# Optimization experiments

Measured on AMD Instinct MI355X. Metric: run time of the kernel, lower is better.

## Reference

```python
import jax, jax.numpy as jnp
import jax.scipy.linalg
import numpy as np
import math

IMG = 512
PATCH = 14
NDIM = 2
HEAD_DIM = 128  # dim // heads = 4096 // 32
STEPS = math.ceil(IMG / PATCH)  # 37


def setup_inputs() -> dict:
    key = jax.random.key(0)
    k1, = jax.random.split(key, 1)
    gen = jax.random.uniform(k1, (NDIM, 1, HEAD_DIM, HEAD_DIM), dtype=jnp.float32) * (2.0 * math.pi)
    image_sizes = jnp.full((1, NDIM), IMG, dtype=jnp.int32)
    return {"image_sizes": image_sizes, "generator_raw_params": gen}


def _positions():
    # cartesian product of linspace(0,1,STEPS) along each axis -> [1, STEPS**NDIM, NDIM]
    axes = [jnp.linspace(0.0, 1.0, STEPS, dtype=jnp.float32) for _ in range(NDIM)]
    grid = jnp.stack(jnp.meshgrid(*axes, indexing="ij"), axis=-1).reshape(-1, NDIM)
    return grid[None]  # [1, N, NDIM]


def reference(image_sizes, generator_raw_params):
    positions = _positions()  # [1, N, NDIM]; image size is static (512) per jit requirements
    upper = jnp.triu(generator_raw_params, k=1) - 0.5  # [NDIM,1,D,D]
    skew = upper - jnp.swapaxes(upper, -1, -2)          # skew-symmetric bases
    # sum over input dims: generator per position, [1, N, 1, D, D]
    gen_pos = jnp.einsum("bnd,dhij->bnhij", positions, skew)
    cls = jnp.zeros_like(gen_pos[:, :1])                # CLS token generator (identity rotation)
    gen_pos = jnp.concatenate([cls, gen_pos], axis=1)   # [1, N+1, 1, D, D]
    b, n, h, d, _ = gen_pos.shape
    flat = gen_pos.astype(jnp.float32).reshape(b * n * h, d, d)
    rot = jax.vmap(jax.scipy.linalg.expm)(flat)
    return rot.reshape(b, n, h, d, d).astype(positions.dtype)
```

## Files before the change

kernel.cpp:

```cpp
#include <hip/hip_runtime.h>
#include <math.h>

#define STEPS 37
#define NMAT  (STEPS*STEPS + 1)
#define D     128
#define NT    512

typedef _Float16 half8 __attribute__((ext_vector_type(8)));
typedef __fp16   fp16x2 __attribute__((ext_vector_type(2)));
typedef float    f32x4 __attribute__((ext_vector_type(4)));

#define PH_OFF   0
#define PL_OFF   32768
#define QTH_OFF  65536
#define QTL_OFF  98304
#define RED_OFF  131072
#define LDS_BYTES (131072 + 640)

__constant__ float dC[8] = {
    1.0f, 1.0f, 5.0e-1f, 1.6666666666666666e-1f, 4.1666666666666664e-2f,
    8.3333333333333332e-3f, 1.3888888888888889e-3f, 1.9841269841269841e-4f };

template<bool WQT, bool WXR, bool WGL>
__device__ __forceinline__ void matmul_step(unsigned char* sm, float diagc,
                                            float* __restrict__ gout,
                                            int wr, int wc, int lr, int g)
{
    f32x4 acc1[4][2] = {};
    f32x4 acc2[4][2] = {};

    #pragma unroll
    for (int ks = 0; ks < 4; ++ks) {
        const int slot = 4*ks + g;
        half8 ah[4], al[4];
        #pragma unroll
        for (int bi = 0; bi < 4; ++bi) {
            const int r = wr*64 + bi*16 + lr;
            const int off = r*256 + ((slot ^ (r & 7)) << 4);
            ah[bi] = *(const half8*)(sm + PH_OFF + off);
            al[bi] = *(const half8*)(sm + PL_OFF + off);
        }
        #pragma unroll
        for (int bj = 0; bj < 2; ++bj) {
            const int c = wc*32 + bj*16 + lr;
            const int off = c*256 + ((slot ^ (c & 7)) << 4);
            const half8 qh = *(const half8*)(sm + QTH_OFF + off);
            const half8 ql = *(const half8*)(sm + QTL_OFF + off);
            #pragma unroll
            for (int bi = 0; bi < 4; ++bi) {
                acc1[bi][bj] = __builtin_amdgcn_mfma_f32_16x16x32_f16(ah[bi], qh, acc1[bi][bj], 0, 0, 0);
                acc2[bi][bj] = __builtin_amdgcn_mfma_f32_16x16x32_f16(ah[bi], ql, acc2[bi][bj], 0, 0, 0);
                acc2[bi][bj] = __builtin_amdgcn_mfma_f32_16x16x32_f16(al[bi], qh, acc2[bi][bj], 0, 0, 0);
            }
        }
    }

    if (WGL) {
        #pragma unroll
        for (int bi = 0; bi < 4; ++bi)
            #pragma unroll
            for (int bj = 0; bj < 2; ++bj) {
                const int col = wc*32 + bj*16 + lr;
                const int r0  = wr*64 + bi*16 + 4*g;
                #pragma unroll
                for (int q = 0; q < 4; ++q)
                    gout[(r0+q)*D + col] = acc1[bi][bj][q] + acc2[bi][bj][q] * (1.0f/2048.0f);
            }
        return;
    }

    uint2 uhv[4][2], ulv[4][2];
    #pragma unroll
    for (int bi = 0; bi < 4; ++bi) {
        #pragma unroll
        for (int bj = 0; bj < 2; ++bj) {
            const int col = wc*32 + bj*16 + lr;
            const int r0  = wr*64 + bi*16 + 4*g;
            float v[4];
            #pragma unroll
            for (int q = 0; q < 4; ++q)
                v[q] = acc1[bi][bj][q] + acc2[bi][bj][q] * (1.0f/2048.0f);
            if (wr*64 + bi*16 == wc*32 + bj*16) {
                #pragma unroll
                for (int q = 0; q < 4; ++q)
                    if (r0 + q == col) v[q] += diagc;
            }
            const fp16x2 h01 = __builtin_amdgcn_cvt_pkrtz(v[0], v[1]);
            const fp16x2 h23 = __builtin_amdgcn_cvt_pkrtz(v[2], v[3]);
            const fp16x2 l01 = __builtin_amdgcn_cvt_pkrtz((v[0]-(float)h01[0])*2048.f,
                                                          (v[1]-(float)h01[1])*2048.f);
            const fp16x2 l23 = __builtin_amdgcn_cvt_pkrtz((v[2]-(float)h23[0])*2048.f,
                                                          (v[3]-(float)h23[1])*2048.f);
            union { fp16x2 h2[2]; uint2 u; } cvh, cvl;
            cvh.h2[0] = h01; cvh.h2[1] = h23;
            cvl.h2[0] = l01; cvl.h2[1] = l23;
            uhv[bi][bj] = cvh.u; ulv[bi][bj] = cvl.u;
        }
    }
    __syncthreads();

    #pragma unroll
    for (int bi = 0; bi < 4; ++bi) {
        #pragma unroll
        for (int bj = 0; bj < 2; ++bj) {
            const int col = wc*32 + bj*16 + lr;
            const int r0  = wr*64 + bi*16 + 4*g;
            if (WQT) {
                const int off = col*256 + (((r0 >> 3) ^ (col & 7)) << 4) + ((g & 1) << 3);
                *(uint2*)(sm + QTH_OFF + off) = uhv[bi][bj];
                *(uint2*)(sm + QTL_OFF + off) = ulv[bi][bj];
            }
            if (WXR) {
                union { uint2 u; _Float16 h[4]; } th, tl;
                th.u = uhv[bi][bj]; tl.u = ulv[bi][bj];
                #pragma unroll
                for (int q = 0; q < 4; ++q) {
                    const int rr = r0 + q;
                    const int off = rr*256 + ((((col >> 3) ^ (rr & 7))) << 4) + ((col & 7) << 1);
                    *(_Float16*)(sm + PH_OFF + off) = th.h[q];
                    *(_Float16*)(sm + PL_OFF + off) = tl.h[q];
                }
            }
        }
    }
    __syncthreads();
}

__global__ __launch_bounds__(NT, 1)
void liere_expm_mfma(const float* __restrict__ gen, float* __restrict__ out)
{
    __shared__ __align__(16) unsigned char sm[LDS_BYTES];
    const int tid = threadIdx.x;
    const int wg  = blockIdx.x;

    float px = 0.f, py = 0.f;
    if (wg > 0) {
        const int idx = wg - 1;
        px = (float)(idx / STEPS) * (1.0f/(STEPS-1));
        py = (float)(idx % STEPS) * (1.0f/(STEPS-1));
    }

    float* Gp = (float*)sm;
    const float* g0 = gen;
    const float* g1 = gen + D*D;
    for (int it = 0; it < 32; ++it) {
        const int e = tid + (it << 9);
        const int i = e >> 7, j = e & 127;
        if (i < j) {
            const float v = px*g0[e] + py*g1[e];
            Gp[i*132 + j] =  v;
            Gp[j*132 + i] = -v;
        } else if (i == j) {
            Gp[i*132 + j] = 0.f;
        }
    }
    __syncthreads();

    float* red = (float*)(sm + RED_OFF);
    if (tid < D) {
        float s = 0.f;
        const f32x4* rowp = (const f32x4*)&Gp[tid*132];
        #pragma unroll 8
        for (int u = 0; u < 32; ++u) {
            const f32x4 v = rowp[u];
            s += fabsf(v.x) + fabsf(v.y) + fabsf(v.z) + fabsf(v.w);
        }
        red[tid] = s;
    }
    __syncthreads();
    #pragma unroll
    for (int off = 64; off >= 1; off >>= 1) {
        if (tid < off) red[tid] = fmaxf(red[tid], red[tid + off]);
        __syncthreads();
    }
    const float m = red[0];
    int nsq = 0;
    if (m > 0.5f) nsq = (int)ceilf(log2f(m * 2.0f));
    if (nsq < 0) nsq = 0;
    const float scale = exp2f(-(float)nsq);

    float vst[32];
    #pragma unroll
    for (int it = 0; it < 32; ++it) {
        const int e = tid + (it << 9);
        vst[it] = Gp[(e>>7)*132 + (e&127)];
    }
    __syncthreads();

    {
        const float c7 = dC[7], c6 = dC[6];
        #pragma unroll
        for (int it = 0; it < 32; ++it) {
            const int e = tid + (it << 9);
            const int i = e >> 7, j = e & 127;
            const float p = vst[it] * scale;
            const _Float16 ph = (_Float16)p;
            const _Float16 pl = (_Float16)((p - (float)ph) * 2048.f);
            const int offP = i*256 + (((j >> 3) ^ (i & 7)) << 4) + ((j & 7) << 1);
            *(_Float16*)(sm + PH_OFF + offP) = ph;
            *(_Float16*)(sm + PL_OFF + offP) = pl;
            const float x = c7*p + ((i == j) ? c6 : 0.f);
            const _Float16 xh = (_Float16)x;
            const _Float16 xl = (_Float16)((x - (float)xh) * 2048.f);
            const int offQ = j*256 + (((i >> 3) ^ (j & 7)) << 4) + ((i & 7) << 1);
            *(_Float16*)(sm + QTH_OFF + offQ) = xh;
            *(_Float16*)(sm + QTL_OFF + offQ) = xl;
        }
    }
    __syncthreads();

    const int lid = tid & 63;
    const int wid = tid >> 6;
    const int wr = wid >> 2, wc = wid & 3;
    const int lr = lid & 15, g = lid >> 4;
    float* gout = out + (size_t)wg * (D*D);

    for (int kk = 5; kk >= 1; --kk)
        matmul_step<true, false, false>(sm, dC[kk], gout, wr, wc, lr, g);
    matmul_step<true, true, false>(sm, dC[0], gout, wr, wc, lr, g);

    if (nsq == 0) {
        for (int it = 0; it < 32; ++it) {
            const int e = tid + (it << 9);
            const int i = e >> 7, j = e & 127;
            const int off = i*256 + (((j >> 3) ^ (i & 7)) << 4) + ((j & 7) << 1);
            gout[e] = (float)*(_Float16*)(sm + PH_OFF + off)
                    + (float)*(_Float16*)(sm + PL_OFF + off) * (1.0f/2048.0f);
        }
        return;
    }

    for (int t = 0; t < nsq - 1; ++t)
        matmul_step<true, true, false>(sm, 0.f, gout, wr, wc, lr, g);
    matmul_step<false, false, true>(sm, 0.f, gout, wr, wc, lr, g);
}

extern "C" void kernel_launch(void* const* d_in, const int* in_sizes, int n_in,
                              void* d_out, int out_size, void* d_ws, size_t ws_size,
                              hipStream_t stream) {
    (void)in_sizes; (void)n_in; (void)d_ws; (void)ws_size; (void)out_size;
    const float* gen = (const float*)d_in[1];
    float* out = (float*)d_out;
    liere_expm_mfma<<<NMAT, NT, 0, stream>>>(gen, out);
}
```

Before: 465.6 us.

## Use 1024-thread blocks, keep P in registers, and ping-pong Horner buffers

Doubles the block to 16 waves, so each wave computes a 32x32 output tile instead of 64x32. The scaled generator P is loaded once into registers and reused across all Horner steps, which removes the repeated LDS reads of the A operand. The Horner Q operand now alternates between two LDS buffers, which drops one barrier per step except the last. In exchange it raises thread count and register pressure per block, and each wave does less MFMA work per barrier.

```diff
diff --git a/kernel.cpp b/kernel.cpp
--- a/kernel.cpp
+++ b/kernel.cpp
@@ -4,129 +4,188 @@
 #define STEPS 37
 #define NMAT  (STEPS*STEPS + 1)
 #define D     128
-#define NT    512
+#define NT    1024
 
 typedef _Float16 half8 __attribute__((ext_vector_type(8)));
 typedef __fp16   fp16x2 __attribute__((ext_vector_type(2)));
 typedef float    f32x4 __attribute__((ext_vector_type(4)));
 
-#define PH_OFF   0
-#define PL_OFF   32768
-#define QTH_OFF  65536
-#define QTL_OFF  98304
-#define RED_OFF  131072
+#define R0H 0
+#define R0L 32768
+#define R1H 65536
+#define R1L 98304
+#define RED_OFF 131072
 #define LDS_BYTES (131072 + 640)
 
 __constant__ float dC[8] = {
     1.0f, 1.0f, 5.0e-1f, 1.6666666666666666e-1f, 4.1666666666666664e-2f,
     8.3333333333333332e-3f, 1.3888888888888889e-3f, 1.9841269841269841e-4f };
 
-template<bool WQT, bool WXR, bool WGL>
-__device__ __forceinline__ void matmul_step(unsigned char* sm, float diagc,
-                                            float* __restrict__ gout,
+__device__ __forceinline__ int swzA(int r, int slot) {
+    return r*256 + ((slot ^ (r & 7)) << 4);
+}
+__device__ __forceinline__ int swzE(int r, int c) {
+    return r*256 + (((c >> 3) ^ (r & 7)) << 4) + ((c & 7) << 1);
+}
+
+__device__ __forceinline__ void conv_tile(const f32x4 a1, const f32x4 a2,
+                                          float diagc, bool hasdiag,
+                                          int r0, int col, uint2& uh, uint2& ul)
+{
+    float v[4];
+    #pragma unroll
+    for (int q = 0; q < 4; ++q) v[q] = a1[q] + a2[q] * (1.0f/2048.0f);
+    if (hasdiag) {
+        #pragma unroll
+        for (int q = 0; q < 4; ++q) if (r0 + q == col) v[q] += diagc;
+    }
+    const fp16x2 h01 = __builtin_amdgcn_cvt_pkrtz(v[0], v[1]);
+    const fp16x2 h23 = __builtin_amdgcn_cvt_pkrtz(v[2], v[3]);
+    const fp16x2 l01 = __builtin_amdgcn_cvt_pkrtz((v[0]-(float)h01[0])*2048.f,
+                                                  (v[1]-(float)h01[1])*2048.f);
+    const fp16x2 l23 = __builtin_amdgcn_cvt_pkrtz((v[2]-(float)h23[0])*2048.f,
+                                                  (v[3]-(float)h23[1])*2048.f);
+    union { fp16x2 h2[2]; uint2 u; } ch, cl;
+    ch.h2[0] = h01; ch.h2[1] = h23;
+    cl.h2[0] = l01; cl.h2[1] = l23;
+    uh = ch.u; ul = cl.u;
+}
+
+template<bool LAST>
+__device__ __forceinline__ void horner_step(unsigned char* sm,
+                                            int srcH, int srcL, int dstH, int dstL,
+                                            const half8 (&pah)[2][4], const half8 (&pal)[2][4],
+                                            float diagc, int wr, int wc, int lr, int g)
+{
+    f32x4 acc1[2][2] = {};
+    f32x4 acc2[2][2] = {};
+    #pragma unroll
+    for (int ks = 0; ks < 4; ++ks) {
+        const int slot = 4*ks + g;
+        #pragma unroll
+        for (int bj = 0; bj < 2; ++bj) {
+            const int c = wc*32 + bj*16 + lr;
+            const int off = swzA(c, slot);
+            const half8 qh = *(const half8*)(sm + srcH + off);
+            const half8 ql = *(const half8*)(sm + srcL + off);
+            #pragma unroll
+            for (int bi = 0; bi < 2; ++bi) {
+                acc1[bi][bj] = __builtin_amdgcn_mfma_f32_16x16x32_f16(pah[bi][ks], qh, acc1[bi][bj], 0, 0, 0);
+                acc2[bi][bj] = __builtin_amdgcn_mfma_f32_16x16x32_f16(pah[bi][ks], ql, acc2[bi][bj], 0, 0, 0);
+                acc2[bi][bj] = __builtin_amdgcn_mfma_f32_16x16x32_f16(pal[bi][ks], qh, acc2[bi][bj], 0, 0, 0);
+            }
+        }
+    }
+    uint2 uh[2][2], ul[2][2];
+    #pragma unroll
+    for (int bi = 0; bi < 2; ++bi)
+        #pragma unroll
+        for (int bj = 0; bj < 2; ++bj) {
+            const int col = wc*32 + bj*16 + lr;
+            const int r0  = wr*32 + bi*16 + 4*g;
+            conv_tile(acc1[bi][bj], acc2[bi][bj], diagc,
+                      wr*32 + bi*16 == wc*32 + bj*16, r0, col, uh[bi][bj], ul[bi][bj]);
+        }
+    if (LAST) __syncthreads();
+    #pragma unroll
+    for (int bi = 0; bi < 2; ++bi)
+        #pragma unroll
+        for (int bj = 0; bj < 2; ++bj) {
+            const int col = wc*32 + bj*16 + lr;
+            const int r0  = wr*32 + bi*16 + 4*g;
+            const int offQ = col*256 + (((r0 >> 3) ^ (col & 7)) << 4) + ((g & 1) << 3);
+            *(uint2*)(sm + dstH + offQ) = uh[bi][bj];
+            *(uint2*)(sm + dstL + offQ) = ul[bi][bj];
+            if (LAST) {
+                union { uint2 u; _Float16 h[4]; } th, tl;
+                th.u = uh[bi][bj]; tl.u = ul[bi][bj];
+                #pragma unroll
+                for (int q = 0; q < 4; ++q) {
+                    const int off = swzE(r0 + q, col);
+                    *(_Float16*)(sm + srcH + off) = th.h[q];
+                    *(_Float16*)(sm + srcL + off) = tl.h[q];
+                }
+            }
+        }
+    __syncthreads();
+}
+
+template<bool WGL>
+__device__ __forceinline__ void square_step(unsigned char* sm, float* __restrict__ gout,
                                             int wr, int wc, int lr, int g)
 {
-    f32x4 acc1[4][2] = {};
-    f32x4 acc2[4][2] = {};
-
+    f32x4 acc1[2][2] = {};
+    f32x4 acc2[2][2] = {};
     #pragma unroll
     for (int ks = 0; ks < 4; ++ks) {
         const int slot = 4*ks + g;
-        half8 ah[4], al[4];
-        #pragma unroll
-        for (int bi = 0; bi < 4; ++bi) {
-            const int r = wr*64 + bi*16 + lr;
-            const int off = r*256 + ((slot ^ (r & 7)) << 4);
-            ah[bi] = *(const half8*)(sm + PH_OFF + off);
-            al[bi] = *(const half8*)(sm + PL_OFF + off);
+        half8 ah[2], al[2];
+        #pragma unroll
+        for (int bi = 0; bi < 2; ++bi) {
+            const int r = wr*32 + bi*16 + lr;
+            const int off = swzA(r, slot);
+            ah[bi] = *(const half8*)(sm + R0H + off);
+            al[bi] = *(const half8*)(sm + R0L + off);
         }
         #pragma unroll
         for (int bj = 0; bj < 2; ++bj) {
             const int c = wc*32 + bj*16 + lr;
-            const int off = c*256 + ((slot ^ (c & 7)) << 4);
-            const half8 qh = *(const half8*)(sm + QTH_OFF + off);
-            const half8 ql = *(const half8*)(sm + QTL_OFF + off);
+            const int off = swzA(c, slot);
+            const half8 qh = *(const half8*)(sm + R1H + off);
+            const half8 ql = *(const half8*)(sm + R1L + off);
             #pragma unroll
-            for (int bi = 0; bi < 4; ++bi) {
+            for (int bi = 0; bi < 2; ++bi) {
                 acc1[bi][bj] = __builtin_amdgcn_mfma_f32_16x16x32_f16(ah[bi], qh, acc1[bi][bj], 0, 0, 0);
                 acc2[bi][bj] = __builtin_amdgcn_mfma_f32_16x16x32_f16(ah[bi], ql, acc2[bi][bj], 0, 0, 0);
                 acc2[bi][bj] = __builtin_amdgcn_mfma_f32_16x16x32_f16(al[bi], qh, acc2[bi][bj], 0, 0, 0);
             }
         }
     }
-
     if (WGL) {
         #pragma unroll
-        for (int bi = 0; bi < 4; ++bi)
+        for (int bi = 0; bi < 2; ++bi)
             #pragma unroll
             for (int bj = 0; bj < 2; ++bj) {
                 const int col = wc*32 + bj*16 + lr;
-                const int r0  = wr*64 + bi*16 + 4*g;
+                const int r0  = wr*32 + bi*16 + 4*g;
                 #pragma unroll
                 for (int q = 0; q < 4; ++q)
                     gout[(r0+q)*D + col] = acc1[bi][bj][q] + acc2[bi][bj][q] * (1.0f/2048.0f);
             }
         return;
     }
-
-    uint2 uhv[4][2], ulv[4][2];
-    #pragma unroll
-    for (int bi = 0; bi < 4; ++bi) {
+    uint2 uh[2][2], ul[2][2];
+    #pragma unroll
+    for (int bi = 0; bi < 2; ++bi)
         #pragma unroll
         for (int bj = 0; bj < 2; ++bj) {
             const int col = wc*32 + bj*16 + lr;
-            const int r0  = wr*64 + bi*16 + 4*g;
-            float v[4];
+            const int r0  = wr*32 + bi*16 + 4*g;
+            conv_tile(acc1[bi][bj], acc2[bi][bj], 0.f, false, r0, col, uh[bi][bj], ul[bi][bj]);
+        }
+    __syncthreads();
+    #pragma unroll
+    for (int bi = 0; bi < 2; ++bi)
+        #pragma unroll
+        for (int bj = 0; bj < 2; ++bj) {
+            const int col = wc*32 + bj*16 + lr;
+            const int r0  = wr*32 + bi*16 + 4*g;
+            const int offQ = col*256 + (((r0 >> 3) ^ (col & 7)) << 4) + ((g & 1) << 3);
+            *(uint2*)(sm + R1H + offQ) = uh[bi][bj];
+            *(uint2*)(sm + R1L + offQ) = ul[bi][bj];
+            union { uint2 u; _Float16 h[4]; } th, tl;
+            th.u = uh[bi][bj]; tl.u = ul[bi][bj];
             #pragma unroll
-            for (int q = 0; q < 4; ++q)
-                v[q] = acc1[bi][bj][q] + acc2[bi][bj][q] * (1.0f/2048.0f);
-            if (wr*64 + bi*16 == wc*32 + bj*16) {
-                #pragma unroll
-                for (int q = 0; q < 4; ++q)
-                    if (r0 + q == col) v[q] += diagc;
-            }
-            const fp16x2 h01 = __builtin_amdgcn_cvt_pkrtz(v[0], v[1]);
-            const fp16x2 h23 = __builtin_amdgcn_cvt_pkrtz(v[2], v[3]);
-            const fp16x2 l01 = __builtin_amdgcn_cvt_pkrtz((v[0]-(float)h01[0])*2048.f,
-                                                          (v[1]-(float)h01[1])*2048.f);
-            const fp16x2 l23 = __builtin_amdgcn_cvt_pkrtz((v[2]-(float)h23[0])*2048.f,
-                                                          (v[3]-(float)h23[1])*2048.f);
-            union { fp16x2 h2[2]; uint2 u; } cvh, cvl;
-            cvh.h2[0] = h01; cvh.h2[1] = h23;
-            cvl.h2[0] = l01; cvl.h2[1] = l23;
-            uhv[bi][bj] = cvh.u; ulv[bi][bj] = cvl.u;
-        }
-    }
-    __syncthreads();
-
-    #pragma unroll
-    for (int bi = 0; bi < 4; ++bi) {
-        #pragma unroll
-        for (int bj = 0; bj < 2; ++bj) {
-            const int col = wc*32 + bj*16 + lr;
-            const int r0  = wr*64 + bi*16 + 4*g;
-            if (WQT) {
-                const int off = col*256 + (((r0 >> 3) ^ (col & 7)) << 4) + ((g & 1) << 3);
-                *(uint2*)(sm + QTH_OFF + off) = uhv[bi][bj];
-                *(uint2*)(sm + QTL_OFF + off) = ulv[bi][bj];
-            }
-            if (WXR) {
-                union { uint2 u; _Float16 h[4]; } th, tl;
-                th.u = uhv[bi][bj]; tl.u = ulv[bi][bj];
-                #pragma unroll
-                for (int q = 0; q < 4; ++q) {
-                    const int rr = r0 + q;
-                    const int off = rr*256 + ((((col >> 3) ^ (rr & 7))) << 4) + ((col & 7) << 1);
-                    *(_Float16*)(sm + PH_OFF + off) = th.h[q];
-                    *(_Float16*)(sm + PL_OFF + off) = tl.h[q];
-                }
-            }
-        }
-    }
-    __syncthreads();
-}
-
-__global__ __launch_bounds__(NT, 1)
+            for (int q = 0; q < 4; ++q) {
+                const int off = swzE(r0 + q, col);
+                *(_Float16*)(sm + R0H + off) = th.h[q];
+                *(_Float16*)(sm + R0L + off) = tl.h[q];
+            }
+        }
+    __syncthreads();
+}
+
+__global__ __launch_bounds__(NT, 4)
 void liere_expm_mfma(const float* __restrict__ gen, float* __restrict__ out)
 {
     __shared__ __align__(16) unsigned char sm[LDS_BYTES];
@@ -143,8 +202,9 @@
     float* Gp = (float*)sm;
     const float* g0 = gen;
     const float* g1 = gen + D*D;
-    for (int it = 0; it < 32; ++it) {
-        const int e = tid + (it << 9);
+    #pragma unroll
+    for (int it = 0; it < 16; ++it) {
+        const int e = tid + (it << 10);
         const int i = e >> 7, j = e & 127;
         if (i < j) {
             const float v = px*g0[e] + py*g1[e];
@@ -179,10 +239,10 @@
     if (nsq < 0) nsq = 0;
     const float scale = exp2f(-(float)nsq);
 
-    float vst[32];
-    #pragma unroll
-    for (int it = 0; it < 32; ++it) {
-        const int e = tid + (it << 9);
+    float vst[16];
+    #pragma unroll
+    for (int it = 0; it < 16; ++it) {
+        const int e = tid + (it << 10);
         vst[it] = Gp[(e>>7)*132 + (e&127)];
     }
     __syncthreads();
@@ -190,21 +250,21 @@
     {
         const float c7 = dC[7], c6 = dC[6];
         #pragma unroll
-        for (int it = 0; it < 32; ++it) {
-            const int e = tid + (it << 9);
+        for (int it = 0; it < 16; ++it) {
+            const int e = tid + (it << 10);
             const int i = e >> 7, j = e & 127;
             const float p = vst[it] * scale;
             const _Float16 ph = (_Float16)p;
             const _Float16 pl = (_Float16)((p - (float)ph) * 2048.f);
-            const int offP = i*256 + (((j >> 3) ^ (i & 7)) << 4) + ((j & 7) << 1);
-            *(_Float16*)(sm + PH_OFF + offP) = ph;
-            *(_Float16*)(sm + PL_OFF + offP) = pl;
+            const int offP = swzE(i, j);
+            *(_Float16*)(sm + R0H + offP) = ph;
+            *(_Float16*)(sm + R0L + offP) = pl;
             const float x = c7*p + ((i == j) ? c6 : 0.f);
             const _Float16 xh = (_Float16)x;
             const _Float16 xl = (_Float16)((x - (float)xh) * 2048.f);
-            const int offQ = j*256 + (((i >> 3) ^ (j & 7)) << 4) + ((i & 7) << 1);
-            *(_Float16*)(sm + QTH_OFF + offQ) = xh;
-            *(_Float16*)(sm + QTL_OFF + offQ) = xl;
+            const int offQ = swzE(j, i);
+            *(_Float16*)(sm + R1H + offQ) = xh;
+            *(_Float16*)(sm + R1L + offQ) = xl;
         }
     }
     __syncthreads();
@@ -215,24 +275,42 @@
     const int lr = lid & 15, g = lid >> 4;
     float* gout = out + (size_t)wg * (D*D);
 
-    for (int kk = 5; kk >= 1; --kk)
-        matmul_step<true, false, false>(sm, dC[kk], gout, wr, wc, lr, g);
-    matmul_step<true, true, false>(sm, dC[0], gout, wr, wc, lr, g);
+    half8 pah[2][4], pal[2][4];
+    #pragma unroll
+    for (int bi = 0; bi < 2; ++bi)
+        #pragma unroll
+        for (int ks = 0; ks < 4; ++ks) {
+            const int r = wr*32 + bi*16 + lr;
+            const int off = swzA(r, 4*ks + g);
+            pah[bi][ks] = *(const half8*)(sm + R0H + off);
+            pal[bi][ks] = *(const half8*)(sm + R0L + off);
+        }
+    __syncthreads();
+
+    int srcH = R1H, srcL = R1L, dstH = R0H, dstL = R0L;
+    for (int kk = 5; kk >= 1; --kk) {
+        horner_step<false>(sm, srcH, srcL, dstH, dstL, pah, pal, dC[kk], wr, wc, lr, g);
+        int t;
+        t = srcH; srcH = dstH; dstH = t;
+        t = srcL; srcL = dstL; dstL = t;
+    }
+    horner_step<true>(sm, srcH, srcL, dstH, dstL, pah, pal, dC[0], wr, wc, lr, g);
 
     if (nsq == 0) {
-        for (int it = 0; it < 32; ++it) {
-            const int e = tid + (it << 9);
+        #pragma unroll
+        for (int it = 0; it < 16; ++it) {
+            const int e = tid + (it << 10);
             const int i = e >> 7, j = e & 127;
-            const int off = i*256 + (((j >> 3) ^ (i & 7)) << 4) + ((j & 7) << 1);
-            gout[e] = (float)*(_Float16*)(sm + PH_OFF + off)
-                    + (float)*(_Float16*)(sm + PL_OFF + off) * (1.0f/2048.0f);
+            const int off = swzE(i, j);
+            gout[e] = (float)*(_Float16*)(sm + R0H + off)
+                    + (float)*(_Float16*)(sm + R0L + off) * (1.0f/2048.0f);
         }
         return;
     }
 
     for (int t = 0; t < nsq - 1; ++t)
-        matmul_step<true, true, false>(sm, 0.f, gout, wr, wc, lr, g);
-    matmul_step<false, false, true>(sm, 0.f, gout, wr, wc, lr, g);
+        square_step<false>(sm, gout, wr, wc, lr, g);
+    square_step<true>(sm, gout, wr, wc, lr, g);
 }
 
 extern "C" void kernel_launch(void* const* d_in, const int* in_sizes, int n_in,
```

After: 513.8 us. +10.4%, slower.
